# Kernel tuning notes

Hardware: AMD Instinct MI355X
Metric: run time of the kernel (lower is better)

The kernel has to match this reference:

```python
import jax, jax.numpy as jnp
import numpy as np

B, S, D_IN, D_ATT = 8, 2048, 512, 512
D_ROT = D_ATT // 2  # RotaryEmbedding(dim=attention_dim//2): only first half of features rotated


def _rotary(x):
    # x: [B, S, D_ATT]; rotate first D_ROT dims with interleaved-pair rotation (lucidrains style)
    seq = x.shape[1]
    inv_freq = 1.0 / (10000.0 ** (jnp.arange(0, D_ROT, 2, dtype=jnp.float32) / D_ROT))  # [D_ROT/2]
    freqs = jnp.arange(seq, dtype=jnp.float32)[:, None] * inv_freq[None, :]             # [S, D_ROT/2]
    freqs = jnp.repeat(freqs, 2, axis=-1)                                               # [S, D_ROT]
    cos, sin = jnp.cos(freqs), jnp.sin(freqs)
    xr = x[..., :D_ROT]
    x1, x2 = xr[..., 0::2], xr[..., 1::2]
    rot = jnp.stack((-x2, x1), axis=-1).reshape(xr.shape)  # rotate_half, interleaved pairs
    return jnp.concatenate([xr * cos + rot * sin, x[..., D_ROT:]], axis=-1)


def setup_inputs() -> dict:
    key = jax.random.key(0)
    ks = jax.random.split(key, 10)
    s = 1.0 / np.sqrt(D_IN)
    return {
        "query": jax.random.normal(ks[0], (B, S, D_IN), dtype=jnp.float32),
        "key": jax.random.normal(ks[1], (B, S, D_IN), dtype=jnp.float32),
        "value": jax.random.normal(ks[2], (B, S, D_IN), dtype=jnp.float32),
        "mask": jax.random.randint(ks[3], (B, S, S), 0, 2, dtype=jnp.int32),
        "Wq": jax.random.uniform(ks[4], (D_IN, D_ATT), jnp.float32, -s, s),
        "bq": jnp.zeros((D_ATT,), jnp.float32),
        "Wk": jax.random.uniform(ks[5], (D_IN, D_ATT), jnp.float32, -s, s),
        "bk": jnp.zeros((D_ATT,), jnp.float32),
        "Wv": jax.random.uniform(ks[6], (D_IN, D_ATT), jnp.float32, -s, s),
        "bv": jnp.zeros((D_ATT,), jnp.float32),
    }


def reference(query, key, value, mask, Wq, bq, Wk, bk, Wv, bv):
    q = query @ Wq + bq
    k = key @ Wk + bk
    v = value @ Wv + bv
    q = _rotary(q)
    k = _rotary(k)
    scores = jnp.einsum("bqd,bkd->bqk", q, k) / jnp.float32(np.sqrt(D_ATT))
    # faithful to source: masked positions get -1e-9 (note: source likely meant -1e9)
    scores = jnp.where(mask == 0, jnp.float32(-1e-9), scores)
    weights = jax.nn.softmax(scores, axis=-1)
    context = jnp.einsum("bqk,bkd->bqd", weights, v)
    return context, weights
```

## Files before the change

### kernel.cpp

```cpp
#include <hip/hip_runtime.h>
#include <hip/hip_bf16.h>

#define B_   8
#define S_   2048
#define DIN  512
#define DATT 512
#define DROT 256

typedef __attribute__((ext_vector_type(4))) float f32x4;
typedef __attribute__((ext_vector_type(8))) short bf16x8;

__device__ __forceinline__ short f2bf(float f) {
    __hip_bfloat16 h = __float2bfloat16(f);
    return *reinterpret_cast<short*>(&h);
}

__global__ void k_tables(float* __restrict__ cosT, float* __restrict__ sinT) {
    int idx = blockIdx.x * 256 + threadIdx.x;
    if (idx >= S_ * 128) return;
    int s = idx >> 7;
    int i = idx & 127;
    float e    = (float)(2 * i) / (float)DROT;
    float invf = 1.0f / powf(10000.0f, e);
    float f    = (float)s * invf;
    float c = cosf(f), sn = sinf(f);
    cosT[s * 256 + 2 * i]     = c;
    cosT[s * 256 + 2 * i + 1] = c;
    sinT[s * 256 + 2 * i]     = sn;
    sinT[s * 256 + 2 * i + 1] = sn;
}

__global__ __launch_bounds__(256) void k_wt(
    const float* __restrict__ Wq, const float* __restrict__ Wk,
    const float* __restrict__ Wv,
    short* __restrict__ WtQ, short* __restrict__ WtK, short* __restrict__ WtV)
{
    const float* W; short* Wt;
    if (blockIdx.y == 0)      { W = Wq; Wt = WtQ; }
    else if (blockIdx.y == 1) { W = Wk; Wt = WtK; }
    else                      { W = Wv; Wt = WtV; }
    int kt = blockIdx.x & 7, nt = blockIdx.x >> 3;
    int k0 = kt * 64, n0 = nt * 64;
    __shared__ float tile[64 * 68];
    int t = threadIdx.x;
    #pragma unroll
    for (int i = 0; i < 4; ++i) {
        int slot = t + 256 * i;
        int row = slot >> 4;
        int c4  = (slot & 15) * 4;
        float4 v = *(const float4*)&W[(size_t)(k0 + row) * DATT + n0 + c4];
        *(float4*)&tile[row * 68 + c4] = v;
    }
    __syncthreads();
    int nr = t >> 2, kq = (t & 3) * 16;
    bf16x8 o0, o1;
    #pragma unroll
    for (int j = 0; j < 8; ++j) o0[j] = f2bf(tile[(kq + j) * 68 + nr]);
    #pragma unroll
    for (int j = 0; j < 8; ++j) o1[j] = f2bf(tile[(kq + 8 + j) * 68 + nr]);
    *(bf16x8*)&Wt[(size_t)(n0 + nr) * DIN + k0 + kq]     = o0;
    *(bf16x8*)&Wt[(size_t)(n0 + nr) * DIN + k0 + kq + 8] = o1;
}

__global__ __launch_bounds__(256) void k_proj(
    const float* __restrict__ X, const short* __restrict__ Wt,
    const float* __restrict__ bias, short* __restrict__ Out,
    const float* __restrict__ cosT, const float* __restrict__ sinT, int doRot)
{
    __shared__ __align__(16) float smem[4608];
    short* As = (short*)smem;
    short* Bs = (short*)(smem + 2560);
    float* Ct = smem;
    int t = threadIdx.x;
    int l = t & 63, w = t >> 6;
    int wr = (w >> 1) * 64, wc = (w & 1) * 64;
    int fr = l & 15, fk = (l >> 4) * 8;
    int rowBase = blockIdx.y * 128;
    int nBase   = blockIdx.x * 128;

    f32x4 acc[4][4] = {};
    int trA = t >> 3, tcA = (t & 7) * 4;
    int srow = w * 16 + (l >> 2), skol = (l & 3) * 8;

    for (int k0 = 0; k0 < DIN; k0 += 32) {
        #pragma unroll
        for (int it = 0; it < 2; ++it) {
            int r = it * 64 + srow;
            __builtin_amdgcn_global_load_lds(
                (const __attribute__((address_space(1))) void*)
                    &Wt[(size_t)(nBase + r) * DIN + k0 + skol],
                (__attribute__((address_space(3))) void*)
                    &Bs[(it * 64 + w * 16) * 32],
                16, 0, 0);
        }
        #pragma unroll
        for (int ii = 0; ii < 4; ++ii) {
            int r = trA + 32 * ii;
            float4 v = *(const float4*)&X[(size_t)(rowBase + r) * DIN + k0 + tcA];
            short4 s4 = make_short4(f2bf(v.x), f2bf(v.y), f2bf(v.z), f2bf(v.w));
            *(short4*)&As[r * 40 + tcA] = s4;
        }
        __syncthreads();
        bf16x8 af[4], bfr[4];
        #pragma unroll
        for (int m = 0; m < 4; ++m)
            af[m] = *(const bf16x8*)&As[(wr + m * 16 + fr) * 40 + fk];
        #pragma unroll
        for (int n = 0; n < 4; ++n)
            bfr[n] = *(const bf16x8*)&Bs[(wc + n * 16 + fr) * 32 + fk];
        #pragma unroll
        for (int m = 0; m < 4; ++m)
            #pragma unroll
            for (int n = 0; n < 4; ++n)
                acc[m][n] = __builtin_amdgcn_mfma_f32_16x16x32_bf16(af[m], bfr[n], acc[m][n], 0, 0, 0);
        __syncthreads();
    }

    for (int ch = 0; ch < 4; ++ch) {
        if ((w & 1) == (ch >> 1)) {
            int nb = (ch & 1) * 2;
            #pragma unroll
            for (int n2 = 0; n2 < 2; ++n2)
                #pragma unroll
                for (int m = 0; m < 4; ++m)
                    #pragma unroll
                    for (int q = 0; q < 4; ++q)
                        Ct[(wr + m * 16 + (l >> 4) * 4 + q) * 34 + n2 * 16 + fr]
                            = acc[m][nb + n2][q];
        }
        __syncthreads();
        {
            int r = t >> 1, seg = (t & 1) * 16;
            int rg = rowBase + r;
            int cg = nBase + ch * 32 + seg;
            float vv[16];
            #pragma unroll
            for (int u = 0; u < 4; ++u)
                *(float4*)&vv[4 * u] = *(float4*)&Ct[r * 34 + seg + 4 * u];
            #pragma unroll
            for (int u = 0; u < 4; ++u) {
                float4 bb = *(const float4*)&bias[cg + 4 * u];
                vv[4 * u + 0] += bb.x; vv[4 * u + 1] += bb.y;
                vv[4 * u + 2] += bb.z; vv[4 * u + 3] += bb.w;
            }
            if (doRot && cg < DROT) {
                int s = rg & (S_ - 1);
                float cs[16], sn[16];
                #pragma unroll
                for (int u = 0; u < 4; ++u) {
                    *(float4*)&cs[4 * u] = *(const float4*)&cosT[s * 256 + cg + 4 * u];
                    *(float4*)&sn[4 * u] = *(const float4*)&sinT[s * 256 + cg + 4 * u];
                }
                #pragma unroll
                for (int j = 0; j < 16; j += 2) {
                    float x1 = vv[j], x2 = vv[j + 1];
                    vv[j]     = x1 * cs[j]     - x2 * sn[j];
                    vv[j + 1] = x2 * cs[j + 1] + x1 * sn[j + 1];
                }
            }
            bf16x8 o0, o1;
            #pragma unroll
            for (int j = 0; j < 8; ++j) { o0[j] = f2bf(vv[j]); o1[j] = f2bf(vv[8 + j]); }
            *(bf16x8*)&Out[(size_t)rg * DATT + cg]     = o0;
            *(bf16x8*)&Out[(size_t)rg * DATT + cg + 8] = o1;
        }
        __syncthreads();
    }
}

__global__ __launch_bounds__(256) void k_vt(
    const short* __restrict__ Vb, short* __restrict__ Vt)
{
    int b = blockIdx.z;
    int d0 = blockIdx.x * 64;
    int r0 = blockIdx.y * 64;
    const short* Vp = Vb + (size_t)b * S_ * DATT;
    short* Tp = Vt + (size_t)b * DATT * S_;
    __shared__ short tile[64 * 66];
    int t = threadIdx.x;
    #pragma unroll
    for (int i = 0; i < 2; ++i) {
        int slot = t + 256 * i;
        int row = slot >> 3;
        int c8  = (slot & 7) * 8;
        bf16x8 v = *(const bf16x8*)&Vp[(size_t)(r0 + row) * DATT + d0 + c8];
        #pragma unroll
        for (int j = 0; j < 8; ++j) tile[row * 66 + c8 + j] = v[j];
    }
    __syncthreads();
    int dr = t >> 2, rq = (t & 3) * 16;
    bf16x8 o0, o1;
    #pragma unroll
    for (int j = 0; j < 8; ++j) o0[j] = tile[(rq + j) * 66 + dr];
    #pragma unroll
    for (int j = 0; j < 8; ++j) o1[j] = tile[(rq + 8 + j) * 66 + dr];
    *(bf16x8*)&Tp[(size_t)(d0 + dr) * S_ + r0 + rq]     = o0;
    *(bf16x8*)&Tp[(size_t)(d0 + dr) * S_ + r0 + rq + 8] = o1;
}

__global__ __launch_bounds__(256) void k_scores(
    const short* __restrict__ Qb, const short* __restrict__ Kb,
    const int* __restrict__ mask, float* __restrict__ wOut)
{
    __shared__ __align__(16) float smem[4352];
    short* As = (short*)smem;
    short* Bs = (short*)(smem + 2048);
    float* Ct = smem;
    int t = threadIdx.x;
    int l = t & 63, w = t >> 6;
    int wr = (w >> 1) * 64, wc = (w & 1) * 64;
    int fr = l & 15, fk = (l >> 4) * 8;
    int b = blockIdx.z;
    int iBase = blockIdx.y * 128;
    int jBase = blockIdx.x * 128;
    const short* Qp = Qb + (size_t)b * S_ * DATT;
    const short* Kp = Kb + (size_t)b * S_ * DATT;

    f32x4 acc[4][4] = {};
    int srow = w * 16 + (l >> 2);
    int skol = (l & 3) * 8;

    for (int k0 = 0; k0 < DATT; k0 += 32) {
        #pragma unroll
        for (int it = 0; it < 2; ++it) {
            int r = it * 64 + srow;
            __builtin_amdgcn_global_load_lds(
                (const __attribute__((address_space(1))) void*)
                    &Qp[(size_t)(iBase + r) * DATT + k0 + skol],
                (__attribute__((address_space(3))) void*)
                    &As[(it * 64 + w * 16) * 32],
                16, 0, 0);
            __builtin_amdgcn_global_load_lds(
                (const __attribute__((address_space(1))) void*)
                    &Kp[(size_t)(jBase + r) * DATT + k0 + skol],
                (__attribute__((address_space(3))) void*)
                    &Bs[(it * 64 + w * 16) * 32],
                16, 0, 0);
        }
        __syncthreads();
        bf16x8 af[4], bfr[4];
        #pragma unroll
        for (int m = 0; m < 4; ++m)
            af[m] = *(const bf16x8*)&As[(wr + m * 16 + fr) * 32 + fk];
        #pragma unroll
        for (int n = 0; n < 4; ++n)
            bfr[n] = *(const bf16x8*)&Bs[(wc + n * 16 + fr) * 32 + fk];
        #pragma unroll
        for (int m = 0; m < 4; ++m)
            #pragma unroll
            for (int n = 0; n < 4; ++n)
                acc[m][n] = __builtin_amdgcn_mfma_f32_16x16x32_bf16(af[m], bfr[n], acc[m][n], 0, 0, 0);
        __syncthreads();
    }

    const float scale = 0.04419417382415922f;
    for (int ch = 0; ch < 4; ++ch) {
        if ((w & 1) == (ch >> 1)) {
            int nb = (ch & 1) * 2;
            #pragma unroll
            for (int n2 = 0; n2 < 2; ++n2)
                #pragma unroll
                for (int m = 0; m < 4; ++m)
                    #pragma unroll
                    for (int q = 0; q < 4; ++q)
                        Ct[(wr + m * 16 + (l >> 4) * 4 + q) * 34 + n2 * 16 + fr]
                            = acc[m][nb + n2][q] * scale;
        }
        __syncthreads();
        {
            int r = t >> 1, seg = (t & 1) * 16;
            int gi = iBase + r;
            size_t base = ((size_t)b * S_ + gi) * S_ + jBase + ch * 32 + seg;
            #pragma unroll
            for (int u = 0; u < 4; ++u) {
                float4 vv = *(float4*)&Ct[r * 34 + seg + 4 * u];
                int4  mm = *(const int4*)&mask[base + 4 * u];
                vv.x = (mm.x == 0) ? -1e-9f : vv.x;
                vv.y = (mm.y == 0) ? -1e-9f : vv.y;
                vv.z = (mm.z == 0) ? -1e-9f : vv.z;
                vv.w = (mm.w == 0) ? -1e-9f : vv.w;
                *(float4*)&wOut[base + 4 * u] = vv;
            }
        }
        __syncthreads();
    }
}

__global__ __launch_bounds__(256) void k_softmax(
    float* __restrict__ wts, short* __restrict__ Pb, int pbe)
{
    size_t row = blockIdx.x;
    float* p = wts + row * S_;
    int t = threadIdx.x, l = t & 63, w = t >> 6;
    float v[8];
    *(float4*)&v[0] = ((const float4*)p)[t];
    *(float4*)&v[4] = ((const float4*)p)[t + 256];
    float mx = v[0];
    #pragma unroll
    for (int j = 1; j < 8; ++j) mx = fmaxf(mx, v[j]);
    for (int off = 32; off; off >>= 1) mx = fmaxf(mx, __shfl_xor(mx, off));
    __shared__ float red[8];
    if (l == 0) red[w] = mx;
    __syncthreads();
    mx = fmaxf(fmaxf(red[0], red[1]), fmaxf(red[2], red[3]));
    float sum = 0.f;
    #pragma unroll
    for (int j = 0; j < 8; ++j) { v[j] = expf(v[j] - mx); sum += v[j]; }
    for (int off = 32; off; off >>= 1) sum += __shfl_xor(sum, off);
    if (l == 0) red[4 + w] = sum;
    __syncthreads();
    sum = red[4] + red[5] + red[6] + red[7];
    float inv = 1.0f / sum;
    #pragma unroll
    for (int j = 0; j < 8; ++j) v[j] *= inv;
    ((float4*)p)[t]       = *(float4*)&v[0];
    ((float4*)p)[t + 256] = *(float4*)&v[4];
    if (pbe) {
        short* pb = Pb + row * S_;
        *(short4*)&pb[4 * t] = make_short4(f2bf(v[0]), f2bf(v[1]), f2bf(v[2]), f2bf(v[3]));
        *(short4*)&pb[1024 + 4 * t] = make_short4(f2bf(v[4]), f2bf(v[5]), f2bf(v[6]), f2bf(v[7]));
    }
}

__global__ __launch_bounds__(256) void k_ctx_bf16(
    const short* __restrict__ Pb, const short* __restrict__ Vt,
    float* __restrict__ ctx)
{
    __shared__ __align__(16) float smem[4352];
    short* As = (short*)smem;
    short* Bs = (short*)(smem + 2048);
    float* Ct = smem;
    int t = threadIdx.x;
    int l = t & 63, w = t >> 6;
    int wr = (w >> 1) * 64, wc = (w & 1) * 64;
    int fr = l & 15, fk = (l >> 4) * 8;
    int b = blockIdx.z;
    int iBase = blockIdx.y * 128;
    int nBase = blockIdx.x * 128;
    const short* Ap = Pb + (size_t)b * S_ * S_;
    const short* Bp = Vt + (size_t)b * DATT * S_;

    f32x4 acc[4][4] = {};
    int srow = w * 16 + (l >> 2);
    int skol = (l & 3) * 8;

    for (int k0 = 0; k0 < S_; k0 += 32) {
        #pragma unroll
        for (int it = 0; it < 2; ++it) {
            int r = it * 64 + srow;
            __builtin_amdgcn_global_load_lds(
                (const __attribute__((address_space(1))) void*)
                    &Ap[(size_t)(iBase + r) * S_ + k0 + skol],
                (__attribute__((address_space(3))) void*)
                    &As[(it * 64 + w * 16) * 32],
                16, 0, 0);
            __builtin_amdgcn_global_load_lds(
                (const __attribute__((address_space(1))) void*)
                    &Bp[(size_t)(nBase + r) * S_ + k0 + skol],
                (__attribute__((address_space(3))) void*)
                    &Bs[(it * 64 + w * 16) * 32],
                16, 0, 0);
        }
        __syncthreads();
        bf16x8 af[4], bfr[4];
        #pragma unroll
        for (int m = 0; m < 4; ++m)
            af[m] = *(const bf16x8*)&As[(wr + m * 16 + fr) * 32 + fk];
        #pragma unroll
        for (int n = 0; n < 4; ++n)
            bfr[n] = *(const bf16x8*)&Bs[(wc + n * 16 + fr) * 32 + fk];
        #pragma unroll
        for (int m = 0; m < 4; ++m)
            #pragma unroll
            for (int n = 0; n < 4; ++n)
                acc[m][n] = __builtin_amdgcn_mfma_f32_16x16x32_bf16(af[m], bfr[n], acc[m][n], 0, 0, 0);
        __syncthreads();
    }

    for (int ch = 0; ch < 4; ++ch) {
        if ((w & 1) == (ch >> 1)) {
            int nb = (ch & 1) * 2;
            #pragma unroll
            for (int n2 = 0; n2 < 2; ++n2)
                #pragma unroll
                for (int m = 0; m < 4; ++m)
                    #pragma unroll
                    for (int q = 0; q < 4; ++q)
                        Ct[(wr + m * 16 + (l >> 4) * 4 + q) * 34 + n2 * 16 + fr]
                            = acc[m][nb + n2][q];
        }
        __syncthreads();
        {
            int r = t >> 1, seg = (t & 1) * 16;
            int gi = iBase + r;
            size_t base = ((size_t)b * S_ + gi) * DATT + nBase + ch * 32 + seg;
            #pragma unroll
            for (int u = 0; u < 4; ++u) {
                float4 vv = *(float4*)&Ct[r * 34 + seg + 4 * u];
                *(float4*)&ctx[base + 4 * u] = vv;
            }
        }
        __syncthreads();
    }
}

__global__ __launch_bounds__(256) void k_ctx_f32(
    const float* __restrict__ wts, const short* __restrict__ Vt,
    float* __restrict__ ctx)
{
    __shared__ short As[128 * 40];
    __shared__ short Bs[128 * 32];
    int t = threadIdx.x;
    int l = t & 63, w = t >> 6;
    int wr = (w >> 1) * 64, wc = (w & 1) * 64;
    int fr = l & 15, fk = (l >> 4) * 8;
    int b = blockIdx.z;
    int iBase = blockIdx.y * 128;
    int nBase = blockIdx.x * 128;
    const float* Wp = wts + (size_t)b * S_ * S_;
    const short* Bp = Vt + (size_t)b * DATT * S_;

    f32x4 acc[4][4] = {};
    int trA = t >> 3, tcA = (t & 7) * 4;
    int srow = w * 16 + (l >> 2), skol = (l & 3) * 8;

    for (int k0 = 0; k0 < S_; k0 += 32) {
        #pragma unroll
        for (int it = 0; it < 2; ++it) {
            int r = it * 64 + srow;
            __builtin_amdgcn_global_load_lds(
                (const __attribute__((address_space(1))) void*)
                    &Bp[(size_t)(nBase + r) * S_ + k0 + skol],
                (__attribute__((address_space(3))) void*)
                    &Bs[(it * 64 + w * 16) * 32],
                16, 0, 0);
        }
        #pragma unroll
        for (int ii = 0; ii < 4; ++ii) {
            int r = trA + 32 * ii;
            float4 v = *(const float4*)&Wp[(size_t)(iBase + r) * S_ + k0 + tcA];
            short4 s4 = make_short4(f2bf(v.x), f2bf(v.y), f2bf(v.z), f2bf(v.w));
            *(short4*)&As[r * 40 + tcA] = s4;
        }
        __syncthreads();
        bf16x8 af[4], bfr[4];
        #pragma unroll
        for (int m = 0; m < 4; ++m)
            af[m] = *(const bf16x8*)&As[(wr + m * 16 + fr) * 40 + fk];
        #pragma unroll
        for (int n = 0; n < 4; ++n)
            bfr[n] = *(const bf16x8*)&Bs[(wc + n * 16 + fr) * 32 + fk];
        #pragma unroll
        for (int m = 0; m < 4; ++m)
            #pragma unroll
            for (int n = 0; n < 4; ++n)
                acc[m][n] = __builtin_amdgcn_mfma_f32_16x16x32_bf16(af[m], bfr[n], acc[m][n], 0, 0, 0);
        __syncthreads();
    }

    for (int m = 0; m < 4; ++m) {
        for (int q = 0; q < 4; ++q) {
            int i = iBase + wr + m * 16 + (l >> 4) * 4 + q;
            for (int n = 0; n < 4; ++n) {
                int d = nBase + wc + n * 16 + fr;
                ctx[((size_t)b * S_ + i) * DATT + d] = acc[m][n][q];
            }
        }
    }
}

extern "C" void kernel_launch(void* const* d_in, const int* in_sizes, int n_in,
                              void* d_out, int out_size, void* d_ws, size_t ws_size,
                              hipStream_t stream) {
    const float* query = (const float*)d_in[0];
    const float* key   = (const float*)d_in[1];
    const float* value = (const float*)d_in[2];
    const int*   mask  = (const int*)d_in[3];
    const float* Wq = (const float*)d_in[4];
    const float* bq = (const float*)d_in[5];
    const float* Wk = (const float*)d_in[6];
    const float* bk = (const float*)d_in[7];
    const float* Wv = (const float*)d_in[8];
    const float* bv = (const float*)d_in[9];

    float* ctx = (float*)d_out;
    float* wts = ctx + (size_t)B_ * S_ * DATT;

    char* ws = (char*)d_ws;
    const size_t SZ_QKV = (size_t)B_ * S_ * DATT * 2;
    const size_t SZ_WT  = (size_t)DATT * DIN * 2;
    const size_t SZ_TAB = (size_t)S_ * 256 * 4;
    short* Qb   = (short*)(ws);
    short* Kb   = (short*)(ws + SZ_QKV);
    short* Vt   = (short*)(ws + 2 * SZ_QKV);
    short* WtQ  = (short*)(ws + 3 * SZ_QKV);
    short* WtK  = (short*)(ws + 3 * SZ_QKV + SZ_WT);
    short* WtV  = (short*)(ws + 3 * SZ_QKV + 2 * SZ_WT);
    float* cosT = (float*)(ws + 3 * SZ_QKV + 3 * SZ_WT);
    float* sinT = (float*)(ws + 3 * SZ_QKV + 3 * SZ_WT + SZ_TAB);
    char*  big  = ws + 3 * SZ_QKV + 3 * SZ_WT + 2 * SZ_TAB;
    short* Vb   = (short*)big;
    short* Pb   = (short*)big;
    const size_t needA = 3 * SZ_QKV + 3 * SZ_WT + 2 * SZ_TAB
                       + (size_t)B_ * S_ * S_ * 2;
    int usePb = ws_size >= needA ? 1 : 0;

    k_tables<<<dim3((S_ * 128) / 256), 256, 0, stream>>>(cosT, sinT);
    k_wt<<<dim3(64, 3), 256, 0, stream>>>(Wq, Wk, Wv, WtQ, WtK, WtV);
    k_proj<<<dim3(4, 128), 256, 0, stream>>>(query, WtQ, bq, Qb, cosT, sinT, 1);
    k_proj<<<dim3(4, 128), 256, 0, stream>>>(key,   WtK, bk, Kb, cosT, sinT, 1);
    k_proj<<<dim3(4, 128), 256, 0, stream>>>(value, WtV, bv, Vb, cosT, sinT, 0);
    k_vt<<<dim3(8, 32, 8), 256, 0, stream>>>(Vb, Vt);
    k_scores<<<dim3(16, 16, 8), 256, 0, stream>>>(Qb, Kb, mask, wts);
    k_softmax<<<dim3(B_ * S_), 256, 0, stream>>>(wts, Pb, usePb);
    if (usePb)
        k_ctx_bf16<<<dim3(4, 16, 8), 256, 0, stream>>>(Pb, Vt, ctx);
    else
        k_ctx_f32<<<dim3(4, 16, 8), 256, 0, stream>>>(wts, Vt, ctx);
}
```

Measured before the change: 593.3 us.

## Stage raw scores in fp16 and move masking into softmax; merge QKV projections

The scores kernel now writes unmasked scaled scores as fp16 into the workspace buffer. Before, it wrote fp32 masked scores to the weights output, which softmax then read back and rewrote. Softmax now reads the fp16 scores and the mask, writes the final fp32 weights once, and overwrites the same buffer in place with bf16 probabilities for the context GEMM. This is meant to cut the fp32 scores round-trip through HBM. The three projection launches are also merged into one launch with a z-dimension. Storing scores in fp16 loses some precision and could overflow for large scores.

```diff
diff --git a/kernel.cpp b/kernel.cpp
--- a/kernel.cpp
+++ b/kernel.cpp
@@ -1,5 +1,6 @@
 #include <hip/hip_runtime.h>
 #include <hip/hip_bf16.h>
+#include <hip/hip_fp16.h>
 
 #define B_   8
 #define S_   2048
@@ -9,10 +10,19 @@
 
 typedef __attribute__((ext_vector_type(4))) float f32x4;
 typedef __attribute__((ext_vector_type(8))) short bf16x8;
+typedef __attribute__((ext_vector_type(8))) unsigned short u16x8;
 
 __device__ __forceinline__ short f2bf(float f) {
     __hip_bfloat16 h = __float2bfloat16(f);
     return *reinterpret_cast<short*>(&h);
+}
+__device__ __forceinline__ unsigned short f2h(float f) {
+    __half h = __float2half(f);
+    return *reinterpret_cast<unsigned short*>(&h);
+}
+__device__ __forceinline__ float h2f(unsigned short u) {
+    __half h = *reinterpret_cast<__half*>(&u);
+    return __half2float(h);
 }
 
 __global__ void k_tables(float* __restrict__ cosT, float* __restrict__ sinT) {
@@ -62,11 +72,21 @@
     *(bf16x8*)&Wt[(size_t)(n0 + nr) * DIN + k0 + kq + 8] = o1;
 }
 
-__global__ __launch_bounds__(256) void k_proj(
-    const float* __restrict__ X, const short* __restrict__ Wt,
-    const float* __restrict__ bias, short* __restrict__ Out,
-    const float* __restrict__ cosT, const float* __restrict__ sinT, int doRot)
-{
+__global__ __launch_bounds__(256) void k_proj3(
+    const float* __restrict__ Xq, const float* __restrict__ Xk,
+    const float* __restrict__ Xv, const short* __restrict__ Wt0,
+    const float* __restrict__ bq, const float* __restrict__ bk,
+    const float* __restrict__ bv,
+    short* __restrict__ Qb, short* __restrict__ Kb, short* __restrict__ Vb,
+    const float* __restrict__ cosT, const float* __restrict__ sinT)
+{
+    int z = blockIdx.z;
+    const float* X    = (z == 0) ? Xq : (z == 1) ? Xk : Xv;
+    const float* bias = (z == 0) ? bq : (z == 1) ? bk : bv;
+    short*       Out  = (z == 0) ? Qb : (z == 1) ? Kb : Vb;
+    const short* Wt   = Wt0 + (size_t)z * DATT * DIN;
+    int doRot = (z < 2);
+
     __shared__ __align__(16) float smem[4608];
     short* As = (short*)smem;
     short* Bs = (short*)(smem + 2560);
@@ -198,9 +218,9 @@
     *(bf16x8*)&Tp[(size_t)(d0 + dr) * S_ + r0 + rq + 8] = o1;
 }
 
-__global__ __launch_bounds__(256) void k_scores(
+__global__ __launch_bounds__(256) void k_scores_h(
     const short* __restrict__ Qb, const short* __restrict__ Kb,
-    const int* __restrict__ mask, float* __restrict__ wOut)
+    unsigned short* __restrict__ Sraw)
 {
     __shared__ __align__(16) float smem[4352];
     short* As = (short*)smem;
@@ -269,32 +289,44 @@
         __syncthreads();
         {
             int r = t >> 1, seg = (t & 1) * 16;
-            int gi = iBase + r;
-            size_t base = ((size_t)b * S_ + gi) * S_ + jBase + ch * 32 + seg;
-            #pragma unroll
-            for (int u = 0; u < 4; ++u) {
-                float4 vv = *(float4*)&Ct[r * 34 + seg + 4 * u];
-                int4  mm = *(const int4*)&mask[base + 4 * u];
-                vv.x = (mm.x == 0) ? -1e-9f : vv.x;
-                vv.y = (mm.y == 0) ? -1e-9f : vv.y;
-                vv.z = (mm.z == 0) ? -1e-9f : vv.z;
-                vv.w = (mm.w == 0) ? -1e-9f : vv.w;
-                *(float4*)&wOut[base + 4 * u] = vv;
-            }
-        }
-        __syncthreads();
-    }
-}
-
-__global__ __launch_bounds__(256) void k_softmax(
-    float* __restrict__ wts, short* __restrict__ Pb, int pbe)
+            size_t base = ((size_t)b * S_ + iBase + r) * S_ + jBase + ch * 32 + seg;
+            float vv[16];
+            #pragma unroll
+            for (int u = 0; u < 4; ++u)
+                *(float4*)&vv[4 * u] = *(float4*)&Ct[r * 34 + seg + 4 * u];
+            u16x8 h0, h1;
+            #pragma unroll
+            for (int j = 0; j < 8; ++j) { h0[j] = f2h(vv[j]); h1[j] = f2h(vv[8 + j]); }
+            *(u16x8*)&Sraw[base]     = h0;
+            *(u16x8*)&Sraw[base + 8] = h1;
+        }
+        __syncthreads();
+    }
+}
+
+__global__ __launch_bounds__(256) void k_softmax_h(
+    unsigned short* __restrict__ SrawPb, const int* __restrict__ mask,
+    float* __restrict__ wts)
 {
     size_t row = blockIdx.x;
-    float* p = wts + row * S_;
+    unsigned short* sp = SrawPb + row * S_;
+    const int* mp = mask + row * S_;
+    float* wp = wts + row * S_;
     int t = threadIdx.x, l = t & 63, w = t >> 6;
+
+    u16x8 raw = *(const u16x8*)&sp[8 * t];
+    int4 m0 = *(const int4*)&mp[8 * t];
+    int4 m1 = *(const int4*)&mp[8 * t + 4];
     float v[8];
-    *(float4*)&v[0] = ((const float4*)p)[t];
-    *(float4*)&v[4] = ((const float4*)p)[t + 256];
+    v[0] = (m0.x == 0) ? -1e-9f : h2f(raw[0]);
+    v[1] = (m0.y == 0) ? -1e-9f : h2f(raw[1]);
+    v[2] = (m0.z == 0) ? -1e-9f : h2f(raw[2]);
+    v[3] = (m0.w == 0) ? -1e-9f : h2f(raw[3]);
+    v[4] = (m1.x == 0) ? -1e-9f : h2f(raw[4]);
+    v[5] = (m1.y == 0) ? -1e-9f : h2f(raw[5]);
+    v[6] = (m1.z == 0) ? -1e-9f : h2f(raw[6]);
+    v[7] = (m1.w == 0) ? -1e-9f : h2f(raw[7]);
+
     float mx = v[0];
     #pragma unroll
     for (int j = 1; j < 8; ++j) mx = fmaxf(mx, v[j]);
@@ -313,13 +345,13 @@
     float inv = 1.0f / sum;
     #pragma unroll
     for (int j = 0; j < 8; ++j) v[j] *= inv;
-    ((float4*)p)[t]       = *(float4*)&v[0];
-    ((float4*)p)[t + 256] = *(float4*)&v[4];
-    if (pbe) {
-        short* pb = Pb + row * S_;
-        *(short4*)&pb[4 * t] = make_short4(f2bf(v[0]), f2bf(v[1]), f2bf(v[2]), f2bf(v[3]));
-        *(short4*)&pb[1024 + 4 * t] = make_short4(f2bf(v[4]), f2bf(v[5]), f2bf(v[6]), f2bf(v[7]));
-    }
+
+    *(float4*)&wp[8 * t]     = make_float4(v[0], v[1], v[2], v[3]);
+    *(float4*)&wp[8 * t + 4] = make_float4(v[4], v[5], v[6], v[7]);
+    bf16x8 pb8;
+    #pragma unroll
+    for (int j = 0; j < 8; ++j) pb8[j] = f2bf(v[j]);
+    *(bf16x8*)&sp[8 * t] = pb8;
 }
 
 __global__ __launch_bounds__(256) void k_ctx_bf16(
@@ -402,6 +434,122 @@
         }
         __syncthreads();
     }
+}
+
+__global__ __launch_bounds__(256) void k_scores_f32(
+    const short* __restrict__ Qb, const short* __restrict__ Kb,
+    const int* __restrict__ mask, float* __restrict__ wOut)
+{
+    __shared__ __align__(16) float smem[4352];
+    short* As = (short*)smem;
+    short* Bs = (short*)(smem + 2048);
+    float* Ct = smem;
+    int t = threadIdx.x;
+    int l = t & 63, w = t >> 6;
+    int wr = (w >> 1) * 64, wc = (w & 1) * 64;
+    int fr = l & 15, fk = (l >> 4) * 8;
+    int b = blockIdx.z;
+    int iBase = blockIdx.y * 128;
+    int jBase = blockIdx.x * 128;
+    const short* Qp = Qb + (size_t)b * S_ * DATT;
+    const short* Kp = Kb + (size_t)b * S_ * DATT;
+
+    f32x4 acc[4][4] = {};
+    int srow = w * 16 + (l >> 2);
+    int skol = (l & 3) * 8;
+
+    for (int k0 = 0; k0 < DATT; k0 += 32) {
+        #pragma unroll
+        for (int it = 0; it < 2; ++it) {
+            int r = it * 64 + srow;
+            __builtin_amdgcn_global_load_lds(
+                (const __attribute__((address_space(1))) void*)
+                    &Qp[(size_t)(iBase + r) * DATT + k0 + skol],
+                (__attribute__((address_space(3))) void*)
+                    &As[(it * 64 + w * 16) * 32],
+                16, 0, 0);
+            __builtin_amdgcn_global_load_lds(
+                (const __attribute__((address_space(1))) void*)
+                    &Kp[(size_t)(jBase + r) * DATT + k0 + skol],
+                (__attribute__((address_space(3))) void*)
+                    &Bs[(it * 64 + w * 16) * 32],
+                16, 0, 0);
+        }
+        __syncthreads();
+        bf16x8 af[4], bfr[4];
+        #pragma unroll
+        for (int m = 0; m < 4; ++m)
+            af[m] = *(const bf16x8*)&As[(wr + m * 16 + fr) * 32 + fk];
+        #pragma unroll
+        for (int n = 0; n < 4; ++n)
+            bfr[n] = *(const bf16x8*)&Bs[(wc + n * 16 + fr) * 32 + fk];
+        #pragma unroll
+        for (int m = 0; m < 4; ++m)
+            #pragma unroll
+            for (int n = 0; n < 4; ++n)
+                acc[m][n] = __builtin_amdgcn_mfma_f32_16x16x32_bf16(af[m], bfr[n], acc[m][n], 0, 0, 0);
+        __syncthreads();
+    }
+
+    const float scale = 0.04419417382415922f;
+    for (int ch = 0; ch < 4; ++ch) {
+        if ((w & 1) == (ch >> 1)) {
+            int nb = (ch & 1) * 2;
+            #pragma unroll
+            for (int n2 = 0; n2 < 2; ++n2)
+                #pragma unroll
+                for (int m = 0; m < 4; ++m)
+                    #pragma unroll
+                    for (int q = 0; q < 4; ++q)
+                        Ct[(wr + m * 16 + (l >> 4) * 4 + q) * 34 + n2 * 16 + fr]
+                            = acc[m][nb + n2][q] * scale;
+        }
+        __syncthreads();
+        {
+            int r = t >> 1, seg = (t & 1) * 16;
+            size_t base = ((size_t)b * S_ + iBase + r) * S_ + jBase + ch * 32 + seg;
+            #pragma unroll
+            for (int u = 0; u < 4; ++u) {
+                float4 vv = *(float4*)&Ct[r * 34 + seg + 4 * u];
+                int4  mm = *(const int4*)&mask[base + 4 * u];
+                vv.x = (mm.x == 0) ? -1e-9f : vv.x;
+                vv.y = (mm.y == 0) ? -1e-9f : vv.y;
+                vv.z = (mm.z == 0) ? -1e-9f : vv.z;
+                vv.w = (mm.w == 0) ? -1e-9f : vv.w;
+                *(float4*)&wOut[base + 4 * u] = vv;
+            }
+        }
+        __syncthreads();
+    }
+}
+
+__global__ __launch_bounds__(256) void k_softmax_f32(float* __restrict__ wts) {
+    size_t row = blockIdx.x;
+    float* p = wts + row * S_;
+    int t = threadIdx.x, l = t & 63, w = t >> 6;
+    float v[8];
+    *(float4*)&v[0] = ((const float4*)p)[t];
+    *(float4*)&v[4] = ((const float4*)p)[t + 256];
+    float mx = v[0];
+    #pragma unroll
+    for (int j = 1; j < 8; ++j) mx = fmaxf(mx, v[j]);
+    for (int off = 32; off; off >>= 1) mx = fmaxf(mx, __shfl_xor(mx, off));
+    __shared__ float red[8];
+    if (l == 0) red[w] = mx;
+    __syncthreads();
+    mx = fmaxf(fmaxf(red[0], red[1]), fmaxf(red[2], red[3]));
+    float sum = 0.f;
+    #pragma unroll
+    for (int j = 0; j < 8; ++j) { v[j] = expf(v[j] - mx); sum += v[j]; }
+    for (int off = 32; off; off >>= 1) sum += __shfl_xor(sum, off);
+    if (l == 0) red[4 + w] = sum;
+    __syncthreads();
+    sum = red[4] + red[5] + red[6] + red[7];
+    float inv = 1.0f / sum;
+    #pragma unroll
+    for (int j = 0; j < 8; ++j) v[j] *= inv;
+    ((float4*)p)[t]       = *(float4*)&v[0];
+    ((float4*)p)[t + 256] = *(float4*)&v[4];
 }
 
 __global__ __launch_bounds__(256) void k_ctx_f32(
@@ -500,21 +648,24 @@
     float* sinT = (float*)(ws + 3 * SZ_QKV + 3 * SZ_WT + SZ_TAB);
     char*  big  = ws + 3 * SZ_QKV + 3 * SZ_WT + 2 * SZ_TAB;
     short* Vb   = (short*)big;
-    short* Pb   = (short*)big;
+    unsigned short* Sraw = (unsigned short*)big;
     const size_t needA = 3 * SZ_QKV + 3 * SZ_WT + 2 * SZ_TAB
                        + (size_t)B_ * S_ * S_ * 2;
-    int usePb = ws_size >= needA ? 1 : 0;
+    int useH = ws_size >= needA ? 1 : 0;
 
     k_tables<<<dim3((S_ * 128) / 256), 256, 0, stream>>>(cosT, sinT);
     k_wt<<<dim3(64, 3), 256, 0, stream>>>(Wq, Wk, Wv, WtQ, WtK, WtV);
-    k_proj<<<dim3(4, 128), 256, 0, stream>>>(query, WtQ, bq, Qb, cosT, sinT, 1);
-    k_proj<<<dim3(4, 128), 256, 0, stream>>>(key,   WtK, bk, Kb, cosT, sinT, 1);
-    k_proj<<<dim3(4, 128), 256, 0, stream>>>(value, WtV, bv, Vb, cosT, sinT, 0);
+    k_proj3<<<dim3(4, 128, 3), 256, 0, stream>>>(query, key, value, WtQ,
+                                                 bq, bk, bv, Qb, Kb, Vb,
+                                                 cosT, sinT);
     k_vt<<<dim3(8, 32, 8), 256, 0, stream>>>(Vb, Vt);
-    k_scores<<<dim3(16, 16, 8), 256, 0, stream>>>(Qb, Kb, mask, wts);
-    k_softmax<<<dim3(B_ * S_), 256, 0, stream>>>(wts, Pb, usePb);
-    if (usePb)
-        k_ctx_bf16<<<dim3(4, 16, 8), 256, 0, stream>>>(Pb, Vt, ctx);
-    else
+    if (useH) {
+        k_scores_h<<<dim3(16, 16, 8), 256, 0, stream>>>(Qb, Kb, Sraw);
+        k_softmax_h<<<dim3(B_ * S_), 256, 0, stream>>>(Sraw, mask, wts);
+        k_ctx_bf16<<<dim3(4, 16, 8), 256, 0, stream>>>((short*)Sraw, Vt, ctx);
+    } else {
+        k_scores_f32<<<dim3(16, 16, 8), 256, 0, stream>>>(Qb, Kb, mask, wts);
+        k_softmax_f32<<<dim3(B_ * S_), 256, 0, stream>>>(wts);
         k_ctx_f32<<<dim3(4, 16, 8), 256, 0, stream>>>(wts, Vt, ctx);
-}
+    }
+}
```

Measured after the change: 542.5 us. 8.6% less time.
